# Kernel optimization log

Measured on AMD Instinct MI355X. Metric: run time of the kernel, lower is better.

The kernel has to match this reference:

```python
import jax, jax.numpy as jnp
import numpy as np

B, T, D = 8, 512, 64

def setup_inputs() -> dict:
    key = jax.random.key(0)
    kx, kw, kb = jax.random.split(key, 3)
    x = jax.random.normal(kx, (B, T, D), dtype=jnp.float32)
    W = jax.random.normal(kw, (D, D), dtype=jnp.float32) / np.sqrt(D)
    b = jax.random.normal(kb, (D,), dtype=jnp.float32) * 0.01
    return {"x": x, "W": W, "b": b}

def reference(x, W, b):
    # v = Linear(x): (B,T,D)
    v = jnp.einsum('btd,ed->bte', x, W) + b
    # pairwise diff: (B,T,T,D); softmax over feature dim D
    diff = x[:, :, None, :] - x[:, None, :, :]
    K = jax.nn.softmax(-(diff * diff), axis=-1)
    # out[b,i,j] = sum_d K[b,i,j,d] * v[b,i,d]  -> (B,T,T)
    out = jnp.einsum('bijd,bid->bij', K, v)
    return out
```

## Files before the change

### kernel.cpp

```cpp
#include <hip/hip_runtime.h>

#define BB 8
#define TT 512
#define DD 64
#define S_SCALE 1.2011224087864498f

typedef float v2f __attribute__((ext_vector_type(2)));
typedef float f8  __attribute__((ext_vector_type(8)));
typedef _Float16 h8 __attribute__((ext_vector_type(8)));

static __device__ __forceinline__ float fast_exp2(float v) {
#if __has_builtin(__builtin_amdgcn_exp2f)
    return __builtin_amdgcn_exp2f(v);
#else
    return exp2f(v);
#endif
}
static __device__ __forceinline__ float fast_rcp(float v) {
#if __has_builtin(__builtin_amdgcn_rcpf)
    return __builtin_amdgcn_rcpf(v);
#else
    return 1.0f / v;
#endif
}
static __device__ __forceinline__ v2f pk_fma(v2f a, v2f b, v2f c) {
#if __has_builtin(__builtin_elementwise_fma)
    return __builtin_elementwise_fma(a, b, c);
#else
    return a * b + c;
#endif
}

__global__ __launch_bounds__(256) void rbf_pre(
    const float* __restrict__ x, const float* __restrict__ W,
    const float* __restrict__ bias,
    _Float16* __restrict__ xh, _Float16* __restrict__ vh)
{
    const int t = threadIdx.x;
    const int w = t >> 6, l = t & 63;
    const int row = blockIdx.x * 4 + w;
    const float* xr = x + (size_t)row * DD;
    const float* wr = W + (size_t)l * DD;
    float acc = bias[l];
    #pragma unroll
    for (int d = 0; d < DD; d += 4) {
        float4 xv = *(const float4*)(xr + d);
        float4 wv = *(const float4*)(wr + d);
        acc = fmaf(xv.x, wv.x, acc); acc = fmaf(xv.y, wv.y, acc);
        acc = fmaf(xv.z, wv.z, acc); acc = fmaf(xv.w, wv.w, acc);
    }
    xh[(size_t)row * DD + l] = (_Float16)(xr[l] * S_SCALE);
    vh[(size_t)row * DD + l] = (_Float16)acc;
}

template <bool MIRROR>
static __device__ __forceinline__ void tile_compute(
    const _Float16* xls, const _Float16* vls,
    const _Float16* xis, const _Float16* vis,
    float* __restrict__ orow0, float* cbuf, int l, int wau)
{
    v2f nr[4][2], nc[4][2], dn[4];
    #pragma unroll
    for (int r = 0; r < 4; ++r) {
        nr[r][0] = (v2f){0.f, 0.f}; nr[r][1] = (v2f){0.f, 0.f};
        nc[r][0] = (v2f){0.f, 0.f}; nc[r][1] = (v2f){0.f, 0.f};
        dn[r]    = (v2f){0.f, 0.f};
    }

    #pragma unroll
    for (int c = 0; c < 8; ++c) {
        h8 xjh = *(const h8*)(xls + l * 72 + c * 8);
        h8 vjh = *(const h8*)(vls + l * 72 + c * 8);
        f8 xj = __builtin_convertvector(xjh, f8);
        f8 vj = __builtin_convertvector(vjh, f8);
        const v2f* xj2 = (const v2f*)&xj;
        const v2f* vj2 = (const v2f*)&vj;
        #pragma unroll
        for (int r = 0; r < 4; ++r) {
            h8 xih = *(const h8*)(xis + (wau * 4 + r) * 72 + c * 8);
            h8 vih = *(const h8*)(vis + (wau * 4 + r) * 72 + c * 8);
            f8 xi = __builtin_convertvector(xih, f8);
            f8 vi = __builtin_convertvector(vih, f8);
            const v2f* xi2 = (const v2f*)&xi;
            const v2f* vi2 = (const v2f*)&vi;
            #pragma unroll
            for (int q = 0; q < 4; ++q) {
                v2f u = xi2[q] - xj2[q];
                u *= u;
                v2f e = {fast_exp2(-u.x), fast_exp2(-u.y)};
                nr[r][q & 1] = pk_fma(e, vi2[q], nr[r][q & 1]);
                if (MIRROR) nc[r][q & 1] = pk_fma(e, vj2[q], nc[r][q & 1]);
                dn[r] += e;
            }
        }
    }

    #pragma unroll
    for (int r = 0; r < 4; ++r) {
        float rd = fast_rcp(dn[r].x + dn[r].y);
        v2f sr = nr[r][0] + nr[r][1];
        orow0[(size_t)r * TT + l] = (sr.x + sr.y) * rd;
        if (MIRROR) {
            v2f sc = nc[r][0] + nc[r][1];
            cbuf[l * 20 + wau * 4 + r] = (sc.x + sc.y) * rd;
        }
    }
}

__global__ __launch_bounds__(256, 4) void rbf_sym(
    const _Float16* __restrict__ xh, const _Float16* __restrict__ vh,
    float* __restrict__ out)
{
    const int bid = blockIdx.x;
    const int b = bid / 144;
    int idx = bid - b * 144;
    int st, jt, isA;
    if (idx < 32) { jt = idx >> 2; st = 4 * jt + (idx & 3); isA = 0; }
    else {
        int k = idx - 32, tt = 1;
        while (k >= 4 * tt) { k -= 4 * tt; ++tt; }
        jt = tt; st = k; isA = 1;
    }
    const int i0 = st * 16, j0 = jt * 64;

    const int tid = threadIdx.x;
    const int w = tid >> 6, l = tid & 63;
    const int wau = __builtin_amdgcn_readfirstlane(w);

    __shared__ __align__(16) _Float16 xls[64 * 72];
    __shared__ __align__(16) _Float16 vls[64 * 72];
    __shared__ __align__(16) _Float16 xis[16 * 72];
    __shared__ __align__(16) _Float16 vis[16 * 72];
    __shared__ float cbuf[64 * 20];

    {
        const uint4* xsrc = (const uint4*)(xh + ((size_t)b * TT + j0) * DD);
        const uint4* vsrc = (const uint4*)(vh + ((size_t)b * TT + j0) * DD);
        #pragma unroll
        for (int u = 0; u < 2; ++u) {
            int g = u * 256 + tid;
            int r = g >> 3, c = g & 7;
            *(uint4*)(xls + r * 72 + c * 8) = xsrc[g];
            *(uint4*)(vls + r * 72 + c * 8) = vsrc[g];
        }
        const uint4* isrc = (tid < 128)
            ? (const uint4*)(xh + ((size_t)b * TT + i0) * DD)
            : (const uint4*)(vh + ((size_t)b * TT + i0) * DD);
        _Float16* idst = (tid < 128) ? xis : vis;
        int g = tid & 127;
        int r = g >> 3, c = g & 7;
        *(uint4*)(idst + r * 72 + c * 8) = isrc[g];
    }
    __syncthreads();

    float* outb  = out + (size_t)b * TT * TT;
    float* orow0 = outb + (size_t)(i0 + wau * 4) * TT + j0;

    if (isA) tile_compute<true >(xls, vls, xis, vis, orow0, cbuf, l, wau);
    else     tile_compute<false>(xls, vls, xis, vis, orow0, cbuf, l, wau);

    __syncthreads();
    if (isA) {
        int j = tid >> 2, qf = (tid & 3) * 4;
        float4 cv = *(const float4*)(cbuf + j * 20 + qf);
        *(float4*)(outb + (size_t)(j0 + j) * TT + i0 + qf) = cv;
    }
}

extern "C" void kernel_launch(void* const* d_in, const int* in_sizes, int n_in,
                              void* d_out, int out_size, void* d_ws, size_t ws_size,
                              hipStream_t stream) {
    const float* x    = (const float*)d_in[0];
    const float* W    = (const float*)d_in[1];
    const float* bias = (const float*)d_in[2];
    float* out        = (float*)d_out;

    _Float16* xh = (_Float16*)d_ws;
    _Float16* vh = (_Float16*)((char*)d_ws + (1 << 19));

    rbf_pre<<<BB * TT / 4, 256, 0, stream>>>(x, W, bias, xh, vh);
    rbf_sym<<<BB * 144, 256, 0, stream>>>(xh, vh, out);
}
```

Measured before the change: 88.67 us.

## Halve row tile to 8 rows, keep i-side operands in fp32 shared memory

Shrinks the i-tile from 16 to 8 rows per block, so each wave handles 2 rows instead of 4. This doubles the block count to 288 per batch and raises the launch-bounds occupancy hint from 4 to 6. The i-side x and v are now loaded from fp32 (x scaled in-kernel, v written by the pre kernel to a new fp32 buffer), which removes the per-row half-to-float conversions in the inner loop. The cost is more blocks, each reloading the 64-row j tile, and fewer i-rows to amortize the xj/vj loads and conversions over.

```diff
diff --git a/kernel.cpp b/kernel.cpp
--- a/kernel.cpp
+++ b/kernel.cpp
@@ -34,7 +34,8 @@
 __global__ __launch_bounds__(256) void rbf_pre(
     const float* __restrict__ x, const float* __restrict__ W,
     const float* __restrict__ bias,
-    _Float16* __restrict__ xh, _Float16* __restrict__ vh)
+    _Float16* __restrict__ xh, _Float16* __restrict__ vh,
+    float* __restrict__ vv)
 {
     const int t = threadIdx.x;
     const int w = t >> 6, l = t & 63;
@@ -51,17 +52,18 @@
     }
     xh[(size_t)row * DD + l] = (_Float16)(xr[l] * S_SCALE);
     vh[(size_t)row * DD + l] = (_Float16)acc;
+    vv[(size_t)row * DD + l] = acc;
 }
 
 template <bool MIRROR>
 static __device__ __forceinline__ void tile_compute(
     const _Float16* xls, const _Float16* vls,
-    const _Float16* xis, const _Float16* vis,
+    const float* xis, const float* vis,
     float* __restrict__ orow0, float* cbuf, int l, int wau)
 {
-    v2f nr[4][2], nc[4][2], dn[4];
+    v2f nr[2][2], nc[2][2], dn[2];
     #pragma unroll
-    for (int r = 0; r < 4; ++r) {
+    for (int r = 0; r < 2; ++r) {
         nr[r][0] = (v2f){0.f, 0.f}; nr[r][1] = (v2f){0.f, 0.f};
         nc[r][0] = (v2f){0.f, 0.f}; nc[r][1] = (v2f){0.f, 0.f};
         dn[r]    = (v2f){0.f, 0.f};
@@ -76,13 +78,9 @@
         const v2f* xj2 = (const v2f*)&xj;
         const v2f* vj2 = (const v2f*)&vj;
         #pragma unroll
-        for (int r = 0; r < 4; ++r) {
-            h8 xih = *(const h8*)(xis + (wau * 4 + r) * 72 + c * 8);
-            h8 vih = *(const h8*)(vis + (wau * 4 + r) * 72 + c * 8);
-            f8 xi = __builtin_convertvector(xih, f8);
-            f8 vi = __builtin_convertvector(vih, f8);
-            const v2f* xi2 = (const v2f*)&xi;
-            const v2f* vi2 = (const v2f*)&vi;
+        for (int r = 0; r < 2; ++r) {
+            const v2f* xi2 = (const v2f*)(xis + (wau * 2 + r) * DD + c * 8);
+            const v2f* vi2 = (const v2f*)(vis + (wau * 2 + r) * DD + c * 8);
             #pragma unroll
             for (int q = 0; q < 4; ++q) {
                 v2f u = xi2[q] - xj2[q];
@@ -96,32 +94,33 @@
     }
 
     #pragma unroll
-    for (int r = 0; r < 4; ++r) {
+    for (int r = 0; r < 2; ++r) {
         float rd = fast_rcp(dn[r].x + dn[r].y);
         v2f sr = nr[r][0] + nr[r][1];
         orow0[(size_t)r * TT + l] = (sr.x + sr.y) * rd;
         if (MIRROR) {
             v2f sc = nc[r][0] + nc[r][1];
-            cbuf[l * 20 + wau * 4 + r] = (sc.x + sc.y) * rd;
+            cbuf[l * 12 + wau * 2 + r] = (sc.x + sc.y) * rd;
         }
     }
 }
 
-__global__ __launch_bounds__(256, 4) void rbf_sym(
+__global__ __launch_bounds__(256, 6) void rbf_sym(
+    const float* __restrict__ x,
     const _Float16* __restrict__ xh, const _Float16* __restrict__ vh,
-    float* __restrict__ out)
+    const float* __restrict__ vv, float* __restrict__ out)
 {
     const int bid = blockIdx.x;
-    const int b = bid / 144;
-    int idx = bid - b * 144;
-    int st, jt, isA;
-    if (idx < 32) { jt = idx >> 2; st = 4 * jt + (idx & 3); isA = 0; }
+    const int b = bid / 288;
+    int idx = bid - b * 288;
+    int ti, jt, isA;
+    if (idx < 64) { jt = idx >> 3; ti = 8 * jt + (idx & 7); isA = 0; }
     else {
-        int k = idx - 32, tt = 1;
-        while (k >= 4 * tt) { k -= 4 * tt; ++tt; }
-        jt = tt; st = k; isA = 1;
+        int k = idx - 64, t = 1;
+        while (k >= 8 * t) { k -= 8 * t; ++t; }
+        jt = t; ti = k; isA = 1;
     }
-    const int i0 = st * 16, j0 = jt * 64;
+    const int i0 = ti * 8, j0 = jt * 64;
 
     const int tid = threadIdx.x;
     const int w = tid >> 6, l = tid & 63;
@@ -129,9 +128,9 @@
 
     __shared__ __align__(16) _Float16 xls[64 * 72];
     __shared__ __align__(16) _Float16 vls[64 * 72];
-    __shared__ __align__(16) _Float16 xis[16 * 72];
-    __shared__ __align__(16) _Float16 vis[16 * 72];
-    __shared__ float cbuf[64 * 20];
+    __shared__ __align__(16) float xis[8 * DD];
+    __shared__ __align__(16) float vis[8 * DD];
+    __shared__ float cbuf[64 * 12];
 
     {
         const uint4* xsrc = (const uint4*)(xh + ((size_t)b * TT + j0) * DD);
@@ -143,26 +142,29 @@
             *(uint4*)(xls + r * 72 + c * 8) = xsrc[g];
             *(uint4*)(vls + r * 72 + c * 8) = vsrc[g];
         }
-        const uint4* isrc = (tid < 128)
-            ? (const uint4*)(xh + ((size_t)b * TT + i0) * DD)
-            : (const uint4*)(vh + ((size_t)b * TT + i0) * DD);
-        _Float16* idst = (tid < 128) ? xis : vis;
         int g = tid & 127;
-        int r = g >> 3, c = g & 7;
-        *(uint4*)(idst + r * 72 + c * 8) = isrc[g];
+        int r = g >> 4, c4 = (g & 15) * 4;
+        if (tid < 128) {
+            float4 v = *(const float4*)(x + ((size_t)(b * TT + i0 + r)) * DD + c4);
+            v.x *= S_SCALE; v.y *= S_SCALE; v.z *= S_SCALE; v.w *= S_SCALE;
+            *(float4*)(xis + r * DD + c4) = v;
+        } else {
+            *(float4*)(vis + r * DD + c4) =
+                *(const float4*)(vv + ((size_t)(b * TT + i0 + r)) * DD + c4);
+        }
     }
     __syncthreads();
 
     float* outb  = out + (size_t)b * TT * TT;
-    float* orow0 = outb + (size_t)(i0 + wau * 4) * TT + j0;
+    float* orow0 = outb + (size_t)(i0 + wau * 2) * TT + j0;
 
     if (isA) tile_compute<true >(xls, vls, xis, vis, orow0, cbuf, l, wau);
     else     tile_compute<false>(xls, vls, xis, vis, orow0, cbuf, l, wau);
 
     __syncthreads();
-    if (isA) {
-        int j = tid >> 2, qf = (tid & 3) * 4;
-        float4 cv = *(const float4*)(cbuf + j * 20 + qf);
+    if (isA && tid < 128) {
+        int j = tid >> 1, qf = (tid & 1) * 4;
+        float4 cv = *(const float4*)(cbuf + j * 12 + qf);
         *(float4*)(outb + (size_t)(j0 + j) * TT + i0 + qf) = cv;
     }
 }
@@ -177,7 +179,8 @@
 
     _Float16* xh = (_Float16*)d_ws;
     _Float16* vh = (_Float16*)((char*)d_ws + (1 << 19));
+    float*    vv = (float*)((char*)d_ws + (1 << 20));
 
-    rbf_pre<<<BB * TT / 4, 256, 0, stream>>>(x, W, bias, xh, vh);
-    rbf_sym<<<BB * 144, 256, 0, stream>>>(xh, vh, out);
+    rbf_pre<<<BB * TT / 4, 256, 0, stream>>>(x, W, bias, xh, vh, vv);
+    rbf_sym<<<BB * 288, 256, 0, stream>>>(x, xh, vh, vv, out);
 }
```

Result: faster. 84.76 us (-4.4%).
